# Optimization experiments

Measured on AMD Instinct MI355X. Metric: run time of the kernel, lower is better.

Reference implementation:

```python
import jax, jax.numpy as jnp
from jax import lax
import numpy as np

H = 16  # GRU hidden = 4**N_GRAM * 4
V = 4   # 4**N_GRAM
B = 512
S = 8192


def _gru_cell(x, h, Wih, Whh, bih, bhh):
    # PyTorch GRU gate ordering: r, z, n
    gi = x @ Wih.T + bih          # [B, 3H]
    gh = h @ Whh.T + bhh          # [B, 3H]
    ir, iz, inn = jnp.split(gi, 3, axis=-1)
    hr, hz, hn = jnp.split(gh, 3, axis=-1)
    r = jax.nn.sigmoid(ir + hr)
    z = jax.nn.sigmoid(iz + hz)
    n = jnp.tanh(inn + r * hn)
    return (1.0 - z) * n + z * h


def setup_inputs() -> dict:
    key = jax.random.key(0)
    ks = jax.random.split(key, 12)
    f32 = jnp.float32
    k_i = 1.0 / np.sqrt(H)  # torch default GRU/Linear init scale
    u = lambda k, shp: jax.random.uniform(k, shp, f32, -k_i, k_i)
    gt = jax.random.normal(ks[0], (B, V, S), f32)
    return {
        "ground_truth": gt,
        "enc_Wih": u(ks[1], (3 * H, V)),
        "enc_Whh": u(ks[2], (3 * H, H)),
        "enc_bih": u(ks[3], (3 * H,)),
        "enc_bhh": u(ks[4], (3 * H,)),
        "dec_Wih": u(ks[5], (3 * H, V)),
        "dec_Whh": u(ks[6], (3 * H, H)),
        "dec_bih": u(ks[7], (3 * H,)),
        "dec_bhh": u(ks[8], (3 * H,)),
        "out_W": u(ks[9], (V, H)),
        "out_b": u(ks[10], (V,)),
        "emb": jnp.eye(V, dtype=f32),  # one-hot Embedding_LUT (frozen)
        "tf_rate": 1,
    }


def reference(ground_truth, enc_Wih, enc_Whh, enc_bih, enc_bhh,
              dec_Wih, dec_Whh, dec_bih, dec_bhh, out_W, out_b, emb, tf_rate):
    gt = jnp.transpose(ground_truth, (2, 0, 1))      # [S, B, V]
    seq_l, batch, _ = gt.shape
    dt = gt.dtype
    h0 = jnp.zeros((batch, H), dt)

    def enc_step(h, x):
        return _gru_cell(x, h, enc_Wih, enc_Whh, enc_bih, enc_bhh), None
    enc_hidden, _ = lax.scan(enc_step, h0, gt)

    targets = jnp.argmax(gt, axis=2)                 # [S, B] int
    x0 = jnp.zeros((batch, V), dt)
    loss0 = jnp.asarray(0.0, dt)

    if tf_rate >= 1:  # argmax-feedback branch (random() < tf_rate always true)
        def dec_step(carry, tgt):
            x, h, loss = carry
            h = _gru_cell(x, h, dec_Wih, dec_Whh, dec_bih, dec_bhh)
            out = h @ out_W.T + out_b                # [B, V]
            logp = jax.nn.log_softmax(out, axis=-1)
            nll = -jnp.mean(jnp.take_along_axis(logp, tgt[:, None], axis=1))
            top_i = jnp.argmax(out, axis=-1)
            return (emb[top_i], h, loss + nll), None
        (_, _, loss), _ = lax.scan(dec_step, (x0, enc_hidden, loss0), targets)
        output_batch = jnp.zeros((seq_l, batch, V), dt)  # never written in this branch
    else:  # teacher-forcing branch (NLLLoss applied to raw logits, as in source)
        def dec_step(carry, inp):
            x, h, loss = carry
            gt_t, tgt = inp
            h = _gru_cell(x, h, dec_Wih, dec_Whh, dec_bih, dec_bhh)
            out = h @ out_W.T + out_b
            nll = -jnp.mean(jnp.take_along_axis(out, tgt[:, None], axis=1))
            return (gt_t, h, loss + nll), out
        (_, _, loss), output_batch = lax.scan(dec_step, (x0, enc_hidden, loss0), (gt, targets))

    return loss, jnp.transpose(output_batch, (1, 2, 0))  # [B, V, S]
```

## Files before the change

### kernel.cpp

```cpp
#include <hip/hip_runtime.h>

#define S_LEN 8192
#define NH 16
#define NV 4
#define NB 512

typedef _Float16 h2 __attribute__((ext_vector_type(2)));

#define L2E  1.4426950408889634f
#define L2E2 2.8853900817779268f

template<int R>
__device__ __forceinline__ float rotf(float v) {
    return __int_as_float(__builtin_amdgcn_mov_dpp(__float_as_int(v), 0x120 + R, 0xF, 0xF, true));
}
template<int R>
__device__ __forceinline__ h2 roth(h2 v) {
    int i;
    __builtin_memcpy(&i, &v, 4);
    i = __builtin_amdgcn_mov_dpp(i, 0x120 + R, 0xF, 0xF, true);
    h2 o;
    __builtin_memcpy(&o, &i, 4);
    return o;
}
__device__ __forceinline__ float qxor1(float v) {
    return __int_as_float(__builtin_amdgcn_mov_dpp(__float_as_int(v), 0xB1, 0xF, 0xF, true));
}
__device__ __forceinline__ float qxor2(float v) {
    return __int_as_float(__builtin_amdgcn_mov_dpp(__float_as_int(v), 0x4E, 0xF, 0xF, true));
}

__device__ __forceinline__ float fex2(float x) { return __builtin_amdgcn_exp2f(x); }
__device__ __forceinline__ float frcp(float x) { return __builtin_amdgcn_rcpf(x); }
__device__ __forceinline__ float fsig2(float x) { return frcp(1.0f + fex2(-x)); }
__device__ __forceinline__ float4 ld4(const float* p) { return *(const float4*)p; }

__device__ __forceinline__ h2 pkh(float a, float b) {
    auto t = __builtin_amdgcn_cvt_pkrtz(a, b);
    h2 o;
    __builtin_memcpy(&o, &t, 4);
    return o;
}

__device__ __forceinline__ void bcast32(float v, float& lo, float& hi) {
    lo = v; hi = v;
    asm("v_permlane32_swap_b32 %0, %1" : "+v"(lo), "+v"(hi));
}

#define FILL_HP16(hp, h)                                      \
    do {                                                      \
        h2 p0_ = pkh((h), rotf<1>(h));                        \
        hp[0] = p0_;                                          \
        hp[1] = roth<2>(p0_);                                 \
        hp[2] = roth<4>(p0_);                                 \
        hp[3] = roth<6>(p0_);                                 \
        hp[4] = roth<8>(p0_);                                 \
        hp[5] = roth<10>(p0_);                                \
        hp[6] = roth<12>(p0_);                                \
        hp[7] = roth<14>(p0_);                                \
    } while (0)

__device__ __forceinline__ float dotd2(const h2* __restrict__ w, const h2* hp, float start) {
    float a = __builtin_amdgcn_fdot2(w[0], hp[0], start, false);
    float b = __builtin_amdgcn_fdot2(w[1], hp[1], 0.0f, false);
    a = __builtin_amdgcn_fdot2(w[2], hp[2], a, false);
    b = __builtin_amdgcn_fdot2(w[3], hp[3], b, false);
    a = __builtin_amdgcn_fdot2(w[4], hp[4], a, false);
    b = __builtin_amdgcn_fdot2(w[5], hp[5], b, false);
    a = __builtin_amdgcn_fdot2(w[6], hp[6], a, false);
    b = __builtin_amdgcn_fdot2(w[7], hp[7], b, false);
    return a + b;
}
__device__ __forceinline__ float dotd2x(const h2* __restrict__ w, const h2* hp, float start) {
    float a = __builtin_amdgcn_fdot2(w[0], hp[0], start, false);
    float b = __builtin_amdgcn_fdot2(w[1], hp[1], 0.0f, false);
    a = __builtin_amdgcn_fdot2(w[2], hp[2], a, false);
    b = __builtin_amdgcn_fdot2(w[3], hp[3], b, false);
    a = __builtin_amdgcn_fdot2(w[4], hp[4], a, false);
    b = __builtin_amdgcn_fdot2(w[5], hp[5], b, false);
    a = __builtin_amdgcn_fdot2(w[6], hp[6], a, false);
    b = __builtin_amdgcn_fdot2(w[7], hp[7], b, false);
    a = __builtin_amdgcn_fdot2(w[8], hp[8], a, false);
    b = __builtin_amdgcn_fdot2(w[9], hp[9], b, false);
    return a + b;
}

__global__ __launch_bounds__(64, 1) void enc_kernel(
    const float* __restrict__ gt,
    const float* __restrict__ eWih, const float* __restrict__ eWhh,
    const float* __restrict__ ebih, const float* __restrict__ ebhh,
    float* __restrict__ hsc)
{
    const int lane = threadIdx.x;
    const int j    = lane & 15;
    const int row  = lane >> 4;
    const bool isLo = (lane < 32);
    const int b    = blockIdx.x * 2 + (row & 1);

    int probe = __builtin_amdgcn_mov_dpp(j, 0x121, 0xF, 0xF, true);
    const int sgn = (probe == ((j + 1) & 15)) ? 1 : -1;

    const float* gb = gt + (size_t)b * (NV * S_LEN);

    const int gA = isLo ? 0 : 1;
    h2 wA[10], wB[10];
#pragma unroll
    for (int p = 0; p < 8; ++p) {
        int k0 = (j + sgn * (2 * p)) & 15;
        int k1 = (j + sgn * (2 * p + 1)) & 15;
        wA[p] = (h2){(_Float16)(L2E * eWhh[(gA * NH + j) * NH + k0]),
                     (_Float16)(L2E * eWhh[(gA * NH + j) * NH + k1])};
        float n0 = isLo ? (L2E2 * eWhh[(2 * NH + j) * NH + k0]) : 0.0f;
        float n1 = isLo ? (L2E2 * eWhh[(2 * NH + j) * NH + k1]) : 0.0f;
        wB[p] = (h2){(_Float16)n0, (_Float16)n1};
    }
#pragma unroll
    for (int p = 0; p < 2; ++p) {
        wA[8 + p] = (h2){(_Float16)(L2E * eWih[(gA * NH + j) * NV + 2 * p]),
                         (_Float16)(L2E * eWih[(gA * NH + j) * NV + 2 * p + 1])};
        float n0 = isLo ? 0.0f : (L2E2 * eWih[(2 * NH + j) * NV + 2 * p]);
        float n1 = isLo ? 0.0f : (L2E2 * eWih[(2 * NH + j) * NV + 2 * p + 1]);
        wB[8 + p] = (h2){(_Float16)n0, (_Float16)n1};
    }
    const float startA = L2E * (ebih[gA * NH + j] + ebhh[gA * NH + j]);
    const float startB = isLo ? (L2E2 * ebhh[2 * NH + j]) : (L2E2 * ebih[2 * NH + j]);

    float h = 0.0f;

    auto estep = [&](float x0, float x1, float x2, float x3) {
        h2 hp[10];
        FILL_HP16(hp, h);
        hp[8] = pkh(x0, x1);
        hp[9] = pkh(x2, x3);
        float vA = dotd2x(wA, hp, startA);
        float vB = dotd2x(wB, hp, startB);
        float ar, az, hn, inn;
        bcast32(vA, ar, az);
        bcast32(vB, hn, inn);
        float r  = fsig2(ar);
        float z  = fsig2(az);
        float y  = fmaf(r, hn, inn);
        float w2 = fsig2(y);
        float t2 = fmaf(-2.0f, z, 2.0f);
        float tb = fmaf(z, h, z - 1.0f);
        h = fmaf(w2, t2, tb);
    };

    {
        float4 A0 = ld4(gb + 0 * S_LEN), A1 = ld4(gb + 1 * S_LEN),
               A2 = ld4(gb + 2 * S_LEN), A3 = ld4(gb + 3 * S_LEN);
        float4 B0 = ld4(gb + 0 * S_LEN + 4), B1 = ld4(gb + 1 * S_LEN + 4),
               B2 = ld4(gb + 2 * S_LEN + 4), B3 = ld4(gb + 3 * S_LEN + 4);
        for (int t = 0; t < S_LEN; t += 8) {
            estep(A0.x, A1.x, A2.x, A3.x);
            estep(A0.y, A1.y, A2.y, A3.y);
            estep(A0.z, A1.z, A2.z, A3.z);
            estep(A0.w, A1.w, A2.w, A3.w);
            int ta = t + 8;  if (ta > S_LEN - 4) ta = S_LEN - 4;
            A0 = ld4(gb + 0 * S_LEN + ta); A1 = ld4(gb + 1 * S_LEN + ta);
            A2 = ld4(gb + 2 * S_LEN + ta); A3 = ld4(gb + 3 * S_LEN + ta);
            estep(B0.x, B1.x, B2.x, B3.x);
            estep(B0.y, B1.y, B2.y, B3.y);
            estep(B0.z, B1.z, B2.z, B3.z);
            estep(B0.w, B1.w, B2.w, B3.w);
            int tb2 = t + 12; if (tb2 > S_LEN - 4) tb2 = S_LEN - 4;
            B0 = ld4(gb + 0 * S_LEN + tb2); B1 = ld4(gb + 1 * S_LEN + tb2);
            B2 = ld4(gb + 2 * S_LEN + tb2); B3 = ld4(gb + 3 * S_LEN + tb2);
        }
    }

    if (isLo) hsc[(size_t)b * NH + j] = h;
}

__global__ __launch_bounds__(64, 1) void dec_kernel(
    const float* __restrict__ dWih, const float* __restrict__ dWhh,
    const float* __restrict__ dbih, const float* __restrict__ dbhh,
    const float* __restrict__ oW,  const float* __restrict__ ob,
    const float* __restrict__ hsc,
    float* __restrict__ outs)
{
    const int lane = threadIdx.x;
    const int j    = lane & 15;
    const int q    = j & 3;
    const int row  = lane >> 4;
    const bool isLo = (lane < 32);
    const int b    = blockIdx.x * 2 + (row & 1);

    int probe = __builtin_amdgcn_mov_dpp(j, 0x121, 0xF, 0xF, true);
    const int sgn = (probe == ((j + 1) & 15)) ? 1 : -1;

    const int gA = isLo ? 0 : 1;
    h2 wA[8], wB[8];
#pragma unroll
    for (int p = 0; p < 8; ++p) {
        int k0 = (j + sgn * (2 * p)) & 15;
        int k1 = (j + sgn * (2 * p + 1)) & 15;
        wA[p] = (h2){(_Float16)(L2E * dWhh[(gA * NH + j) * NH + k0]),
                     (_Float16)(L2E * dWhh[(gA * NH + j) * NH + k1])};
        float w0 = isLo ? (L2E2 * dWhh[(2 * NH + j) * NH + k0]) : oW[q * NH + k0];
        float w1 = isLo ? (L2E2 * dWhh[(2 * NH + j) * NH + k1]) : oW[q * NH + k1];
        wB[p] = (h2){(_Float16)w0, (_Float16)w1};
    }
    const float bNi  = dbih[2 * NH + j];
    const float bNiS = L2E2 * bNi;
    const float biasA  = L2E * (dbih[gA * NH + j] + dbhh[gA * NH + j]);
    const float startB = isLo ? (L2E2 * dbhh[2 * NH + j]) : ob[q];
    float SA[NV], KN[NV];
#pragma unroll
    for (int m = 0; m < NV; ++m) {
        int c = m ^ q;
        SA[m] = L2E * dWih[(gA * NH + j) * NV + c];
        KN[m] = L2E2 * (bNi + dWih[(2 * NH + j) * NV + c]);
    }

    float h = hsc[(size_t)b * NH + j];

    int oidx = (b << 15) + q;
    const bool storer = isLo && (j < 4);

    auto dstep = [&]() {
        h2 hp[8];
        FILL_HP16(hp, h);
        float aA = dotd2(wA, hp, biasA);
        float vB = dotd2(wB, hp, startB);
        float hn, oa;
        bcast32(vB, hn, oa);
        if (storer) outs[oidx] = oa;
        oidx += 4;
        float ob_ = qxor1(oa);
        float oc_ = qxor2(oa);
        float od_ = qxor2(ob_);
        bool cA = ob_ > oa;  float mA = fmaxf(oa, ob_);
        bool cB = od_ > oc_; float mB = fmaxf(oc_, od_);
        bool hi_ = mB > mA;
        float KA  = hi_ ? (cB ? SA[3] : SA[2]) : (cA ? SA[1] : SA[0]);
        float KN_ = hi_ ? (cB ? KN[3] : KN[2]) : (cA ? KN[1] : KN[0]);
        float sg  = fsig2(aA + KA);
        float r, z;
        bcast32(sg, r, z);
        float y   = fmaf(r, hn, KN_);
        float w2  = fsig2(y);
        float t2  = fmaf(-2.0f, z, 2.0f);
        float tb  = fmaf(z, h, z - 1.0f);
        h = fmaf(w2, t2, tb);
    };

    {
        h2 hp[8];
        FILL_HP16(hp, h);
        float aA = dotd2(wA, hp, biasA);
        float vB = dotd2(wB, hp, startB);
        float hn, oa;
        bcast32(vB, hn, oa);
        float sg = fsig2(aA);
        float r, z;
        bcast32(sg, r, z);
        float y  = fmaf(r, hn, bNiS);
        float w2 = fsig2(y);
        float t2 = fmaf(-2.0f, z, 2.0f);
        float tb = fmaf(z, h, z - 1.0f);
        h = fmaf(w2, t2, tb);
    }
    for (int u = 0; u < S_LEN - 4; u += 4) {
        dstep(); dstep(); dstep(); dstep();
    }
    dstep(); dstep(); dstep();

    {
        h2 hp[8];
        FILL_HP16(hp, h);
        float vB = dotd2(wB, hp, startB);
        float hn, oa;
        bcast32(vB, hn, oa);
        if (storer) outs[oidx] = oa;
    }
}

__global__ __launch_bounds__(1024) void loss_kernel(
    const float* __restrict__ gt, float* __restrict__ outs, float* __restrict__ loss)
{
    int tid = blockIdx.x * 1024 + threadIdx.x;
    int t = tid & (S_LEN - 1);
    int b = tid >> 13;
    float4 o = *(const float4*)(outs + (size_t)tid * 4);
    const float* g = gt + (size_t)b * (NV * S_LEN) + t;
    float p0 = g[0], p1 = g[S_LEN], p2 = g[2 * S_LEN], p3 = g[3 * S_LEN];
    int tg = (p1 > p0) ? 1 : 0;  float bm = fmaxf(p0, p1);
    tg = (p2 > bm) ? 2 : tg;     bm = fmaxf(p2, bm);
    tg = (p3 > bm) ? 3 : tg;
    float vt = (tg & 1) ? ((tg & 2) ? o.w : o.y) : ((tg & 2) ? o.z : o.x);
    float mx = fmaxf(fmaxf(o.x, o.y), fmaxf(o.z, o.w));
    float ss = __expf(o.x - mx) + __expf(o.y - mx) + __expf(o.z - mx) + __expf(o.w - mx);
    float v  = (mx - vt) + __logf(ss);
    *(float4*)(outs + (size_t)tid * 4) = make_float4(0.f, 0.f, 0.f, 0.f);
#pragma unroll
    for (int d = 1; d < 64; d <<= 1) v += __shfl_xor(v, d, 64);
    __shared__ float sm[16];
    int w = threadIdx.x >> 6;
    if ((threadIdx.x & 63) == 0) sm[w] = v;
    __syncthreads();
    if (threadIdx.x < 16) {
        float s = sm[threadIdx.x];
#pragma unroll
        for (int d = 1; d < 16; d <<= 1) s += __shfl_xor(s, d, 64);
        if (threadIdx.x == 0) atomicAdd(loss, s * (1.0f / NB));
    }
}

extern "C" void kernel_launch(void* const* d_in, const int* in_sizes, int n_in,
                              void* d_out, int out_size, void* d_ws, size_t ws_size,
                              hipStream_t stream) {
    (void)in_sizes; (void)n_in; (void)ws_size; (void)out_size;
    const float* gt   = (const float*)d_in[0];
    const float* eWih = (const float*)d_in[1];
    const float* eWhh = (const float*)d_in[2];
    const float* ebih = (const float*)d_in[3];
    const float* ebhh = (const float*)d_in[4];
    const float* dWih = (const float*)d_in[5];
    const float* dWhh = (const float*)d_in[6];
    const float* dbih = (const float*)d_in[7];
    const float* dbhh = (const float*)d_in[8];
    const float* oW   = (const float*)d_in[9];
    const float* ob   = (const float*)d_in[10];

    float* out  = (float*)d_out;
    float* outs = out + 1;
    float* hsc  = (float*)d_ws;
    (void)hipMemsetAsync(d_out, 0, sizeof(float), stream);
    enc_kernel<<<NB / 2, 64, 0, stream>>>(gt, eWih, eWhh, ebih, ebhh, hsc);
    dec_kernel<<<NB / 2, 64, 0, stream>>>(dWih, dWhh, dbih, dbhh, oW, ob, hsc, outs);
    loss_kernel<<<(NB * S_LEN) / 1024, 1024, 0, stream>>>(gt, outs, out);
}
```

Baseline: 3.054 ms.

## Fuse encoder and decoder GRU kernels into one persistent kernel

Merges the encoder and decoder kernels into one kernel so the encoder's final hidden state stays in registers rather than going through a workspace buffer, which also removes one kernel launch. The decoder loop is unrolled by 8 with constant store offsets, and the argmax's third neighbour is fetched with a single quad-permute DPP instead of two chained ones, shortening the dependent chain. The bcast32 helper is also restructured. Register pressure may rise because both phases' weights now live in the same kernel, although they are scoped separately.

```diff
diff --git a/kernel.cpp b/kernel.cpp
--- a/kernel.cpp
+++ b/kernel.cpp
@@ -29,6 +29,9 @@
 __device__ __forceinline__ float qxor2(float v) {
     return __int_as_float(__builtin_amdgcn_mov_dpp(__float_as_int(v), 0x4E, 0xF, 0xF, true));
 }
+__device__ __forceinline__ float qxor3(float v) {
+    return __int_as_float(__builtin_amdgcn_mov_dpp(__float_as_int(v), 0x1B, 0xF, 0xF, true));
+}
 
 __device__ __forceinline__ float fex2(float x) { return __builtin_amdgcn_exp2f(x); }
 __device__ __forceinline__ float frcp(float x) { return __builtin_amdgcn_rcpf(x); }
@@ -43,8 +46,9 @@
 }
 
 __device__ __forceinline__ void bcast32(float v, float& lo, float& hi) {
-    lo = v; hi = v;
-    asm("v_permlane32_swap_b32 %0, %1" : "+v"(lo), "+v"(hi));
+    lo = v;
+    asm("v_permlane32_swap_b32 %0, %1" : "+v"(lo), "+v"(v));
+    hi = v;
 }
 
 #define FILL_HP16(hp, h)                                      \
@@ -85,14 +89,18 @@
     return a + b;
 }
 
-__global__ __launch_bounds__(64, 1) void enc_kernel(
+__global__ __launch_bounds__(64, 1) void rnn_kernel(
     const float* __restrict__ gt,
     const float* __restrict__ eWih, const float* __restrict__ eWhh,
     const float* __restrict__ ebih, const float* __restrict__ ebhh,
-    float* __restrict__ hsc)
+    const float* __restrict__ dWih, const float* __restrict__ dWhh,
+    const float* __restrict__ dbih, const float* __restrict__ dbhh,
+    const float* __restrict__ oW,  const float* __restrict__ ob,
+    float* __restrict__ outs)
 {
     const int lane = threadIdx.x;
     const int j    = lane & 15;
+    const int q    = j & 3;
     const int row  = lane >> 4;
     const bool isLo = (lane < 32);
     const int b    = blockIdx.x * 2 + (row & 1);
@@ -100,53 +108,52 @@
     int probe = __builtin_amdgcn_mov_dpp(j, 0x121, 0xF, 0xF, true);
     const int sgn = (probe == ((j + 1) & 15)) ? 1 : -1;
 
-    const float* gb = gt + (size_t)b * (NV * S_LEN);
-
-    const int gA = isLo ? 0 : 1;
-    h2 wA[10], wB[10];
-#pragma unroll
-    for (int p = 0; p < 8; ++p) {
-        int k0 = (j + sgn * (2 * p)) & 15;
-        int k1 = (j + sgn * (2 * p + 1)) & 15;
-        wA[p] = (h2){(_Float16)(L2E * eWhh[(gA * NH + j) * NH + k0]),
-                     (_Float16)(L2E * eWhh[(gA * NH + j) * NH + k1])};
-        float n0 = isLo ? (L2E2 * eWhh[(2 * NH + j) * NH + k0]) : 0.0f;
-        float n1 = isLo ? (L2E2 * eWhh[(2 * NH + j) * NH + k1]) : 0.0f;
-        wB[p] = (h2){(_Float16)n0, (_Float16)n1};
-    }
-#pragma unroll
-    for (int p = 0; p < 2; ++p) {
-        wA[8 + p] = (h2){(_Float16)(L2E * eWih[(gA * NH + j) * NV + 2 * p]),
-                         (_Float16)(L2E * eWih[(gA * NH + j) * NV + 2 * p + 1])};
-        float n0 = isLo ? 0.0f : (L2E2 * eWih[(2 * NH + j) * NV + 2 * p]);
-        float n1 = isLo ? 0.0f : (L2E2 * eWih[(2 * NH + j) * NV + 2 * p + 1]);
-        wB[8 + p] = (h2){(_Float16)n0, (_Float16)n1};
-    }
-    const float startA = L2E * (ebih[gA * NH + j] + ebhh[gA * NH + j]);
-    const float startB = isLo ? (L2E2 * ebhh[2 * NH + j]) : (L2E2 * ebih[2 * NH + j]);
-
     float h = 0.0f;
 
-    auto estep = [&](float x0, float x1, float x2, float x3) {
-        h2 hp[10];
-        FILL_HP16(hp, h);
-        hp[8] = pkh(x0, x1);
-        hp[9] = pkh(x2, x3);
-        float vA = dotd2x(wA, hp, startA);
-        float vB = dotd2x(wB, hp, startB);
-        float ar, az, hn, inn;
-        bcast32(vA, ar, az);
-        bcast32(vB, hn, inn);
-        float r  = fsig2(ar);
-        float z  = fsig2(az);
-        float y  = fmaf(r, hn, inn);
-        float w2 = fsig2(y);
-        float t2 = fmaf(-2.0f, z, 2.0f);
-        float tb = fmaf(z, h, z - 1.0f);
-        h = fmaf(w2, t2, tb);
-    };
-
     {
+        const float* gb = gt + (size_t)b * (NV * S_LEN);
+        const int gA = isLo ? 0 : 1;
+        h2 wA[10], wB[10];
+#pragma unroll
+        for (int p = 0; p < 8; ++p) {
+            int k0 = (j + sgn * (2 * p)) & 15;
+            int k1 = (j + sgn * (2 * p + 1)) & 15;
+            wA[p] = (h2){(_Float16)(L2E * eWhh[(gA * NH + j) * NH + k0]),
+                         (_Float16)(L2E * eWhh[(gA * NH + j) * NH + k1])};
+            float n0 = isLo ? (L2E2 * eWhh[(2 * NH + j) * NH + k0]) : 0.0f;
+            float n1 = isLo ? (L2E2 * eWhh[(2 * NH + j) * NH + k1]) : 0.0f;
+            wB[p] = (h2){(_Float16)n0, (_Float16)n1};
+        }
+#pragma unroll
+        for (int p = 0; p < 2; ++p) {
+            wA[8 + p] = (h2){(_Float16)(L2E * eWih[(gA * NH + j) * NV + 2 * p]),
+                             (_Float16)(L2E * eWih[(gA * NH + j) * NV + 2 * p + 1])};
+            float n0 = isLo ? 0.0f : (L2E2 * eWih[(2 * NH + j) * NV + 2 * p]);
+            float n1 = isLo ? 0.0f : (L2E2 * eWih[(2 * NH + j) * NV + 2 * p + 1]);
+            wB[8 + p] = (h2){(_Float16)n0, (_Float16)n1};
+        }
+        const float startA = L2E * (ebih[gA * NH + j] + ebhh[gA * NH + j]);
+        const float startB = isLo ? (L2E2 * ebhh[2 * NH + j]) : (L2E2 * ebih[2 * NH + j]);
+
+        auto estep = [&](float x0, float x1, float x2, float x3) {
+            h2 hp[10];
+            FILL_HP16(hp, h);
+            hp[8] = pkh(x0, x1);
+            hp[9] = pkh(x2, x3);
+            float vA = dotd2x(wA, hp, startA);
+            float vB = dotd2x(wB, hp, startB);
+            float ar, az, hn, inn;
+            bcast32(vA, ar, az);
+            bcast32(vB, hn, inn);
+            float r  = fsig2(ar);
+            float z  = fsig2(az);
+            float y  = fmaf(r, hn, inn);
+            float w2 = fsig2(y);
+            float t2 = fmaf(-2.0f, z, 2.0f);
+            float tb = fmaf(z, h, z - 1.0f);
+            h = fmaf(w2, t2, tb);
+        };
+
         float4 A0 = ld4(gb + 0 * S_LEN), A1 = ld4(gb + 1 * S_LEN),
                A2 = ld4(gb + 2 * S_LEN), A3 = ld4(gb + 3 * S_LEN);
         float4 B0 = ld4(gb + 0 * S_LEN + 4), B1 = ld4(gb + 1 * S_LEN + 4),
@@ -169,26 +176,6 @@
         }
     }
 
-    if (isLo) hsc[(size_t)b * NH + j] = h;
-}
-
-__global__ __launch_bounds__(64, 1) void dec_kernel(
-    const float* __restrict__ dWih, const float* __restrict__ dWhh,
-    const float* __restrict__ dbih, const float* __restrict__ dbhh,
-    const float* __restrict__ oW,  const float* __restrict__ ob,
-    const float* __restrict__ hsc,
-    float* __restrict__ outs)
-{
-    const int lane = threadIdx.x;
-    const int j    = lane & 15;
-    const int q    = j & 3;
-    const int row  = lane >> 4;
-    const bool isLo = (lane < 32);
-    const int b    = blockIdx.x * 2 + (row & 1);
-
-    int probe = __builtin_amdgcn_mov_dpp(j, 0x121, 0xF, 0xF, true);
-    const int sgn = (probe == ((j + 1) & 15)) ? 1 : -1;
-
     const int gA = isLo ? 0 : 1;
     h2 wA[8], wB[8];
 #pragma unroll
@@ -213,23 +200,20 @@
         KN[m] = L2E2 * (bNi + dWih[(2 * NH + j) * NV + c]);
     }
 
-    float h = hsc[(size_t)b * NH + j];
-
     int oidx = (b << 15) + q;
     const bool storer = isLo && (j < 4);
 
-    auto dstep = [&]() {
+    auto dstep = [&](int koff) {
         h2 hp[8];
         FILL_HP16(hp, h);
         float aA = dotd2(wA, hp, biasA);
         float vB = dotd2(wB, hp, startB);
         float hn, oa;
         bcast32(vB, hn, oa);
-        if (storer) outs[oidx] = oa;
-        oidx += 4;
+        if (storer) outs[oidx + koff] = oa;
         float ob_ = qxor1(oa);
         float oc_ = qxor2(oa);
-        float od_ = qxor2(ob_);
+        float od_ = qxor3(oa);
         bool cA = ob_ > oa;  float mA = fmaxf(oa, ob_);
         bool cB = od_ > oc_; float mB = fmaxf(oc_, od_);
         bool hi_ = mB > mA;
@@ -261,10 +245,14 @@
         float tb = fmaf(z, h, z - 1.0f);
         h = fmaf(w2, t2, tb);
     }
-    for (int u = 0; u < S_LEN - 4; u += 4) {
-        dstep(); dstep(); dstep(); dstep();
-    }
-    dstep(); dstep(); dstep();
+    for (int u = 0; u < 8184; u += 8) {
+#pragma unroll
+        for (int k = 0; k < 8; ++k) dstep(k * 4);
+        oidx += 32;
+    }
+#pragma unroll
+    for (int k = 0; k < 7; ++k) dstep(k * 4);
+    oidx += 28;
 
     {
         h2 hp[8];
@@ -310,7 +298,7 @@
 extern "C" void kernel_launch(void* const* d_in, const int* in_sizes, int n_in,
                               void* d_out, int out_size, void* d_ws, size_t ws_size,
                               hipStream_t stream) {
-    (void)in_sizes; (void)n_in; (void)ws_size; (void)out_size;
+    (void)in_sizes; (void)n_in; (void)d_ws; (void)ws_size; (void)out_size;
     const float* gt   = (const float*)d_in[0];
     const float* eWih = (const float*)d_in[1];
     const float* eWhh = (const float*)d_in[2];
@@ -325,9 +313,8 @@
 
     float* out  = (float*)d_out;
     float* outs = out + 1;
-    float* hsc  = (float*)d_ws;
     (void)hipMemsetAsync(d_out, 0, sizeof(float), stream);
-    enc_kernel<<<NB / 2, 64, 0, stream>>>(gt, eWih, eWhh, ebih, ebhh, hsc);
-    dec_kernel<<<NB / 2, 64, 0, stream>>>(dWih, dWhh, dbih, dbhh, oW, ob, hsc, outs);
+    rnn_kernel<<<NB / 2, 64, 0, stream>>>(gt, eWih, eWhh, ebih, ebhh,
+                                          dWih, dWhh, dbih, dbhh, oW, ob, outs);
     loss_kernel<<<(NB * S_LEN) / 1024, 1024, 0, stream>>>(gt, outs, out);
 }
```

Result: faster. 2.987 ms (-2.2%).
